# Optimization experiments

Measured on AMD Instinct MI355X. Metric: run time of the kernel, lower is better.

The kernel has to match this reference:

```python
import jax, jax.numpy as jnp
import numpy as np

D_MODEL = 1024
N_HEADS = 16
D_HEAD = D_MODEL // N_HEADS

def setup_inputs() -> dict:
    key = jax.random.key(0)
    ks = jax.random.split(key, 5)
    B, T = 4, 2048
    s = 1.0 / np.sqrt(D_MODEL)
    return {
        "x": jax.random.normal(ks[0], (B, T, D_MODEL), dtype=jnp.float32),
        "qkv_w": jax.random.normal(ks[1], (3 * D_MODEL, D_MODEL), dtype=jnp.float32) * s,
        "qkv_b": jnp.zeros((3 * D_MODEL,), dtype=jnp.float32),
        "out_w": jax.random.normal(ks[2], (D_MODEL, D_MODEL), dtype=jnp.float32) * s,
        "out_b": jnp.zeros((D_MODEL,), dtype=jnp.float32),
    }

def reference(x, qkv_w, qkv_b, out_w, out_b):
    B, T, D = x.shape
    # fused QKV projection: [B,T,3D] -> [3,B,H,T,dh]
    qkv = (x @ qkv_w.T + qkv_b).reshape(B, T, 3, N_HEADS, D_HEAD)
    qkv = jnp.transpose(qkv, (2, 0, 3, 1, 4))
    q, k, v = qkv[0], qkv[1], qkv[2]
    scale = 1.0 / np.sqrt(D_HEAD).astype(np.float32)
    scores = jnp.einsum("bhqd,bhkd->bhqk", q, k) * scale
    attn = jax.nn.softmax(scores, axis=-1)
    ctx = jnp.einsum("bhqk,bhkd->bhqd", attn, v)  # [B,H,T,dh]
    ctx = jnp.transpose(ctx, (0, 2, 1, 3)).reshape(B, T, D)
    return ctx @ out_w.T + out_b
```

## Files before the change

kernel.cpp:

```cpp
#include <hip/hip_runtime.h>
#include <hip/hip_bf16.h>
#include <cstdint>
#include <cstddef>


#define SEQ 2048
#define DM 1024

typedef __attribute__((ext_vector_type(8))) short bf16x8;
typedef __attribute__((ext_vector_type(4))) short bf16x4;
typedef __attribute__((ext_vector_type(4))) float f32x4;

static __device__ __forceinline__ short f2bf(float f) {
  union { float f; uint32_t u; } v; v.f = f;
  uint32_t r = v.u + 0x7fffu + ((v.u >> 16) & 1u);
  return (short)(r >> 16);
}

static __device__ __forceinline__ float exp2_native(float x) {
  return __builtin_amdgcn_exp2f(x);
}

typedef const __attribute__((address_space(1))) unsigned int* gas_ptr;
typedef __attribute__((address_space(3))) unsigned int* las_ptr;
static __device__ __forceinline__ void gl2lds16(const void* g, void* l) {
  __builtin_amdgcn_global_load_lds((gas_ptr)g, (las_ptr)l, 16, 0, 0);
}

static __device__ __forceinline__ unsigned permhi(float a_odd, float a_even) {
  union { float f; unsigned u; } x, y; x.f = a_odd; y.f = a_even;
  return __builtin_amdgcn_perm(x.u, y.u, 0x07060302u);
}
static __device__ __forceinline__ bf16x8 pack8t(const float* e) {
  union { bf16x8 v; unsigned u[4]; } r;
  r.u[0] = permhi(e[1], e[0]);
  r.u[1] = permhi(e[3], e[2]);
  r.u[2] = permhi(e[5], e[4]);
  r.u[3] = permhi(e[7], e[6]);
  return r.v;
}

static __device__ __forceinline__ int swz(int r) {
  return (r & 3) | (((r >> 3) & 1) << 2);
}

__global__ __launch_bounds__(256)
void cvt_bf16(const float* __restrict__ src, short* __restrict__ dst) {
  int i = blockIdx.x * 256 + threadIdx.x;
  float4 v = ((const float4*)src)[i];
  bf16x4 p = { f2bf(v.x), f2bf(v.y), f2bf(v.z), f2bf(v.w) };
  ((bf16x4*)dst)[i] = p;
}

__global__ __launch_bounds__(256)
void cvt_bf16_2(const float* __restrict__ src1, short* __restrict__ dst1, int n1,
                const float* __restrict__ src2, short* __restrict__ dst2) {
  int b = blockIdx.x;
  const float* s; short* d; int i;
  if (b < n1) { s = src1; d = dst1; i = b * 256 + threadIdx.x; }
  else        { s = src2; d = dst2; i = (b - n1) * 256 + threadIdx.x; }
  float4 v = ((const float4*)s)[i];
  bf16x4 p = { f2bf(v.x), f2bf(v.y), f2bf(v.z), f2bf(v.w) };
  ((bf16x4*)d)[i] = p;
}

__global__ __launch_bounds__(256)
void cvt_bf16_3(const float* __restrict__ src1, short* __restrict__ dst1, int n1,
                const float* __restrict__ src2, short* __restrict__ dst2, int n2,
                const float* __restrict__ src3, short* __restrict__ dst3) {
  int b = blockIdx.x;
  const float* s; short* d; int i;
  if (b < n1)           { s = src1; d = dst1; i = b * 256 + threadIdx.x; }
  else if (b < n1 + n2) { s = src2; d = dst2; i = (b - n1) * 256 + threadIdx.x; }
  else                  { s = src3; d = dst3; i = (b - n1 - n2) * 256 + threadIdx.x; }
  float4 v = ((const float4*)s)[i];
  bf16x4 p = { f2bf(v.x), f2bf(v.y), f2bf(v.z), f2bf(v.w) };
  ((bf16x4*)d)[i] = p;
}

__global__ __launch_bounds__(256, 2)
void qkv_gemm(const short* __restrict__ Xb, const short* __restrict__ Wb,
              const float* __restrict__ bias,
              short* __restrict__ Q, short* __restrict__ K,
              short* __restrict__ Vt) {
  __shared__ short As[2][128 * 64];
  __shared__ short Bs[2][128 * 64];
  const int tid  = threadIdx.x;
  const int m0   = blockIdx.x * 128;
  const int n0   = blockIdx.y * 128;
  const int lane = tid & 63;
  const int w    = tid >> 6;
  const int wm   = (w >> 1) * 64, wn = (w & 1) * 64;
  const int l15  = lane & 15, quad = lane >> 4;

  int g_row[4], g_col[4];
#pragma unroll
  for (int p = 0; p < 4; p++) {
    int r = p * 32 + w * 8 + (lane >> 3);
    g_row[p] = r;
    g_col[p] = ((lane & 7) ^ swz(r)) << 3;
  }
  int aoff[4][2], boff[4][2];
#pragma unroll
  for (int i = 0; i < 4; i++)
#pragma unroll
    for (int ks = 0; ks < 2; ks++) {
      int Ra = wm + i * 16 + l15;
      aoff[i][ks] = Ra * 128 + (((ks * 4 + quad) ^ swz(Ra)) << 4);
      int Rb = wn + i * 16 + l15;
      boff[i][ks] = Rb * 128 + (((ks * 4 + quad) ^ swz(Rb)) << 4);
    }

  f32x4 acc[4][4];
  for (int i = 0; i < 4; i++)
    for (int j = 0; j < 4; j++) acc[i][j] = (f32x4)0.0f;

#pragma unroll
  for (int p = 0; p < 4; p++) {
    gl2lds16(&Xb[(size_t)(m0 + g_row[p]) * DM + g_col[p]], &As[0][(p * 32 + w * 8) * 64]);
    gl2lds16(&Wb[(size_t)(n0 + g_row[p]) * DM + g_col[p]], &Bs[0][(p * 32 + w * 8) * 64]);
  }

  for (int t = 0; t < 16; t++) {
    const int cur = t & 1;
    if (t + 1 < 16) {
      const int kk = (t + 1) * 64;
#pragma unroll
      for (int p = 0; p < 4; p++) {
        gl2lds16(&Xb[(size_t)(m0 + g_row[p]) * DM + kk + g_col[p]], &As[cur ^ 1][(p * 32 + w * 8) * 64]);
        gl2lds16(&Wb[(size_t)(n0 + g_row[p]) * DM + kk + g_col[p]], &Bs[cur ^ 1][(p * 32 + w * 8) * 64]);
      }
      asm volatile("s_waitcnt vmcnt(8)" ::: "memory");
    } else {
      asm volatile("s_waitcnt vmcnt(0)" ::: "memory");
    }
    __builtin_amdgcn_s_barrier();
    __builtin_amdgcn_sched_barrier(0);

    const char* Ab = (const char*)&As[cur][0];
    const char* Bb = (const char*)&Bs[cur][0];
#pragma unroll
    for (int ks = 0; ks < 2; ks++) {
      bf16x8 af[4], bfr[4];
      for (int i = 0; i < 4; i++) af[i]  = *(const bf16x8*)(Ab + aoff[i][ks]);
      for (int j = 0; j < 4; j++) bfr[j] = *(const bf16x8*)(Bb + boff[j][ks]);
      for (int i = 0; i < 4; i++)
        for (int j = 0; j < 4; j++)
          acc[i][j] = __builtin_amdgcn_mfma_f32_16x16x32_bf16(af[i], bfr[j], acc[i][j], 0, 0, 0);
    }
    __builtin_amdgcn_sched_barrier(0);
    __builtin_amdgcn_s_barrier();
    __builtin_amdgcn_sched_barrier(0);
  }

  const float C1 = 0.18033688011112042f;
  const int qkv = n0 >> 10;
  for (int i = 0; i < 4; i++) {
    const int m = m0 + wm + i * 16 + quad * 4;
    const int bb = m >> 11, t = m & 2047;
    for (int j = 0; j < 4; j++) {
      const int f  = n0 + wn + j * 16 + l15;
      const int fi = f & 1023;
      const int h  = fi >> 6, d = fi & 63;
      const float bv = bias[f];
      if (qkv == 2) {
        bf16x4 pk = { f2bf(acc[i][j][0] + bv), f2bf(acc[i][j][1] + bv),
                      f2bf(acc[i][j][2] + bv), f2bf(acc[i][j][3] + bv) };
        *(bf16x4*)&Vt[((size_t)(bb * 16 + h) * 64 + d) * SEQ + t] = pk;
      } else {
        short* dst = (qkv == 0) ? Q : K;
        const float sc = (qkv == 0) ? C1 : 1.0f;
        size_t base = ((size_t)(bb * 16 + h) * SEQ + t) * 64 + d;
        for (int r = 0; r < 4; r++)
          dst[base + (size_t)r * 64] = f2bf((acc[i][j][r] + bv) * sc);
      }
    }
  }
}

__global__ __launch_bounds__(256, 4)
void attn(const short* __restrict__ Q, const short* __restrict__ K,
          const short* __restrict__ Vt, short* __restrict__ ctx) {
  __shared__ short Ks[2][64 * 64];
  __shared__ short Vs[2][64 * 64];
  const int tid  = threadIdx.x;
  const int w    = tid >> 6, lane = tid & 63;
  const int l15  = lane & 15, quad = lane >> 4;

  const int L    = blockIdx.y * 16 + blockIdx.x;
  const int m_   = L >> 3;
  const int bh   = ((m_ >> 4) << 3) | (L & 7);
  const int qr   = (m_ & 15) * 128 + w * 32;

  const short* Kb = &K[(size_t)bh * SEQ * 64];
  const short* Vb = &Vt[(size_t)bh * 64 * SEQ];

  const int kperm = (l15 >> 2) * 8 + (l15 & 3);

  int dr[2], dc[2];
#pragma unroll
  for (int p = 0; p < 2; p++) {
    int ci = p * 256 + w * 64 + lane;
    dr[p] = ci >> 3;
    dc[p] = (ci & 7) ^ swz(ci >> 3);
  }
  const short* kp[2];
  const short* vp[2];
#pragma unroll
  for (int p = 0; p < 2; p++) {
    kp[p] = &Kb[(size_t)(64 + dr[p]) * 64 + dc[p] * 8];
    vp[p] = &Vb[(size_t)dr[p] * SEQ + 64 + dc[p] * 8];
  }

  int koff[2][2][2][2];
  int voff[2][4][2];
#pragma unroll
  for (int blk = 0; blk < 2; blk++)
#pragma unroll
    for (int tau = 0; tau < 2; tau++)
#pragma unroll
      for (int ks = 0; ks < 2; ks++) {
        int R = blk * 32 + kperm + tau * 4;
        int c = (ks * 4 + quad) ^ swz(R);
        int off = (R * 8 + c) * 16;
        koff[0][blk][tau][ks] = off;
        koff[1][blk][tau][ks] = off + 8192;
      }
#pragma unroll
  for (int dt = 0; dt < 4; dt++)
#pragma unroll
    for (int blk = 0; blk < 2; blk++) {
      int R = dt * 16 + l15;
      int c = (blk * 4 + quad) ^ swz(R);
      int off = (R * 8 + c) * 16;
      voff[0][dt][blk] = off;
      voff[1][dt][blk] = off + 8192;
    }
  const char* KsB = (const char*)&Ks[0][0];
  const char* VsB = (const char*)&Vs[0][0];

  bf16x8 qf[2][2];
#pragma unroll
  for (int mt = 0; mt < 2; mt++)
#pragma unroll
    for (int ks = 0; ks < 2; ks++)
      qf[mt][ks] = *(const bf16x8*)&Q[(size_t)bh * SEQ * 64 + (size_t)(qr + mt * 16 + l15) * 64 + ks * 32 + quad * 8];

  f32x4 O[2][4];
#pragma unroll
  for (int mt = 0; mt < 2; mt++)
    for (int dt = 0; dt < 4; dt++) O[mt][dt] = (f32x4)0.0f;
  f32x4 psA[2];
  psA[0] = (f32x4)0.0f; psA[1] = (f32x4)0.0f;
  const short one_bf = (short)0x3F80;
  const bf16x8 ones = { one_bf, one_bf, one_bf, one_bf, one_bf, one_bf, one_bf, one_bf };

#pragma unroll
  for (int p = 0; p < 2; p++) {
    gl2lds16(&Kb[(size_t)dr[p] * 64 + dc[p] * 8],  &Ks[0][(p * 256 + w * 64) * 8]);
    gl2lds16(&Vb[(size_t)dr[p] * SEQ + dc[p] * 8], &Vs[0][(p * 256 + w * 64) * 8]);
  }
  __syncthreads();

  for (int k0 = 0; k0 < SEQ; k0 += 128) {
#pragma unroll
    for (int half = 0; half < 2; half++) {
      const bool doPf = (half == 0) || (k0 + 128 < SEQ);
      if (doPf) {
#pragma unroll
        for (int p = 0; p < 2; p++) {
          gl2lds16(kp[p], &Ks[half ^ 1][(p * 256 + w * 64) * 8]);
          gl2lds16(vp[p], &Vs[half ^ 1][(p * 256 + w * 64) * 8]);
        }
      }
#pragma unroll
      for (int p = 0; p < 2; p++) { kp[p] += 64 * 64; vp[p] += 64; }

      bf16x8 kf[2][2][2];
#pragma unroll
      for (int blk = 0; blk < 2; blk++)
#pragma unroll
        for (int tau = 0; tau < 2; tau++)
#pragma unroll
          for (int ks = 0; ks < 2; ks++)
            kf[blk][tau][ks] = *(const bf16x8*)(KsB + koff[half][blk][tau][ks]);

      f32x4 S[2][2][2];
#pragma unroll
      for (int mt = 0; mt < 2; mt++)
#pragma unroll
        for (int blk = 0; blk < 2; blk++) {
          f32x4 S0 = (f32x4)0.0f, S1 = (f32x4)0.0f;
#pragma unroll
          for (int ks = 0; ks < 2; ks++) {
            S0 = __builtin_amdgcn_mfma_f32_16x16x32_bf16(kf[blk][0][ks], qf[mt][ks], S0, 0, 0, 0);
            S1 = __builtin_amdgcn_mfma_f32_16x16x32_bf16(kf[blk][1][ks], qf[mt][ks], S1, 0, 0, 0);
          }
          S[mt][blk][0] = S0; S[mt][blk][1] = S1;
        }

      bf16x8 vf[4][2];
#pragma unroll
      for (int dt = 0; dt < 4; dt++)
#pragma unroll
        for (int blk = 0; blk < 2; blk++)
          vf[dt][blk] = *(const bf16x8*)(VsB + voff[half][dt][blk]);

      bf16x8 pp[2][2];
#pragma unroll
      for (int mt = 0; mt < 2; mt++)
#pragma unroll
        for (int blk = 0; blk < 2; blk++) {
          float e[8];
#pragma unroll
          for (int r = 0; r < 4; r++) {
            e[r]     = exp2_native(S[mt][blk][0][r]);
            e[4 + r] = exp2_native(S[mt][blk][1][r]);
          }
          pp[mt][blk] = pack8t(e);
        }

#pragma unroll
      for (int blk = 0; blk < 2; blk++) {
#pragma unroll
        for (int dt = 0; dt < 4; dt++) {
          O[0][dt] = __builtin_amdgcn_mfma_f32_16x16x32_bf16(vf[dt][blk], pp[0][blk], O[0][dt], 0, 0, 0);
          O[1][dt] = __builtin_amdgcn_mfma_f32_16x16x32_bf16(vf[dt][blk], pp[1][blk], O[1][dt], 0, 0, 0);
        }
        psA[0] = __builtin_amdgcn_mfma_f32_16x16x32_bf16(ones, pp[0][blk], psA[0], 0, 0, 0);
        psA[1] = __builtin_amdgcn_mfma_f32_16x16x32_bf16(ones, pp[1][blk], psA[1], 0, 0, 0);
      }

      __syncthreads();
    }
  }

  const int bb = bh >> 4, h = bh & 15;
#pragma unroll
  for (int mt = 0; mt < 2; mt++) {
    float rinv = 1.0f / psA[mt][0];
    const int t = qr + mt * 16 + l15;
#pragma unroll
    for (int dt = 0; dt < 4; dt++) {
      bf16x4 ov = { f2bf(O[mt][dt][0] * rinv), f2bf(O[mt][dt][1] * rinv),
                    f2bf(O[mt][dt][2] * rinv), f2bf(O[mt][dt][3] * rinv) };
      *(bf16x4*)&ctx[(size_t)(bb * SEQ + t) * DM + h * 64 + dt * 16 + quad * 4] = ov;
    }
  }
}

__global__ __launch_bounds__(256, 2)
void out_gemm(const short* __restrict__ Cx, const short* __restrict__ Ob,
              const float* __restrict__ bias, float* __restrict__ Y) {
  __shared__ short As[2][128 * 64];
  __shared__ short Bs[2][128 * 64];
  const int tid  = threadIdx.x;
  const int m0   = blockIdx.x * 128;
  const int n0   = blockIdx.y * 128;
  const int lane = tid & 63;
  const int w    = tid >> 6;
  const int wm   = (w >> 1) * 64, wn = (w & 1) * 64;
  const int l15  = lane & 15, quad = lane >> 4;

  int g_row[4], g_col[4];
#pragma unroll
  for (int p = 0; p < 4; p++) {
    int r = p * 32 + w * 8 + (lane >> 3);
    g_row[p] = r;
    g_col[p] = ((lane & 7) ^ swz(r)) << 3;
  }
  int aoff[4][2], boff[4][2];
#pragma unroll
  for (int i = 0; i < 4; i++)
#pragma unroll
    for (int ks = 0; ks < 2; ks++) {
      int Ra = wm + i * 16 + l15;
      aoff[i][ks] = Ra * 128 + (((ks * 4 + quad) ^ swz(Ra)) << 4);
      int Rb = wn + i * 16 + l15;
      boff[i][ks] = Rb * 128 + (((ks * 4 + quad) ^ swz(Rb)) << 4);
    }

  f32x4 acc[4][4];
  for (int i = 0; i < 4; i++)
    for (int j = 0; j < 4; j++) acc[i][j] = (f32x4)0.0f;

#pragma unroll
  for (int p = 0; p < 4; p++) {
    gl2lds16(&Cx[(size_t)(m0 + g_row[p]) * DM + g_col[p]], &As[0][(p * 32 + w * 8) * 64]);
    gl2lds16(&Ob[(size_t)(n0 + g_row[p]) * DM + g_col[p]], &Bs[0][(p * 32 + w * 8) * 64]);
  }

  for (int t = 0; t < 16; t++) {
    const int cur = t & 1;
    if (t + 1 < 16) {
      const int kk = (t + 1) * 64;
#pragma unroll
      for (int p = 0; p < 4; p++) {
        gl2lds16(&Cx[(size_t)(m0 + g_row[p]) * DM + kk + g_col[p]], &As[cur ^ 1][(p * 32 + w * 8) * 64]);
        gl2lds16(&Ob[(size_t)(n0 + g_row[p]) * DM + kk + g_col[p]], &Bs[cur ^ 1][(p * 32 + w * 8) * 64]);
      }
      asm volatile("s_waitcnt vmcnt(8)" ::: "memory");
    } else {
      asm volatile("s_waitcnt vmcnt(0)" ::: "memory");
    }
    __builtin_amdgcn_s_barrier();
    __builtin_amdgcn_sched_barrier(0);

    const char* Ab = (const char*)&As[cur][0];
    const char* Bb = (const char*)&Bs[cur][0];
#pragma unroll
    for (int ks = 0; ks < 2; ks++) {
      bf16x8 af[4], bfr[4];
      for (int i = 0; i < 4; i++) af[i]  = *(const bf16x8*)(Ab + aoff[i][ks]);
      for (int j = 0; j < 4; j++) bfr[j] = *(const bf16x8*)(Bb + boff[j][ks]);
      for (int i = 0; i < 4; i++)
        for (int j = 0; j < 4; j++)
          acc[i][j] = __builtin_amdgcn_mfma_f32_16x16x32_bf16(af[i], bfr[j], acc[i][j], 0, 0, 0);
    }
    __builtin_amdgcn_sched_barrier(0);
    __builtin_amdgcn_s_barrier();
    __builtin_amdgcn_sched_barrier(0);
  }

  for (int i = 0; i < 4; i++) {
    const int m = m0 + wm + i * 16 + quad * 4;
    for (int j = 0; j < 4; j++) {
      const int n = n0 + wn + j * 16 + l15;
      const float bv = bias[n];
      for (int r = 0; r < 4; r++)
        Y[(size_t)(m + r) * DM + n] = acc[i][j][r] + bv;
    }
  }
}

extern "C" void kernel_launch(void* const* d_in, const int* in_sizes, int n_in,
                              void* d_out, int out_size, void* d_ws, size_t ws_size,
                              hipStream_t stream) {
  const float* x     = (const float*)d_in[0];
  const float* qkv_w = (const float*)d_in[1];
  const float* qkv_b = (const float*)d_in[2];
  const float* out_w = (const float*)d_in[3];
  const float* out_b = (const float*)d_in[4];
  float* out = (float*)d_out;

  const size_t NBH = (size_t)4 * 16 * SEQ * 64;
  short* Q   = (short*)d_ws;
  short* K   = Q + NBH;
  short* Vt  = K + NBH;
  short* ctx = Vt + NBH;
  short* Xb  = ctx;
  short* Wb  = (short*)d_out;

  const size_t used  = 4 * NBH * sizeof(short);
  const size_t obsz  = (size_t)DM * DM * sizeof(short);
  const bool   bigws = ws_size >= used + obsz;

  if (bigws) {
    short* Ob = (short*)((char*)d_ws + used);
    cvt_bf16_3<<<dim3(8192 + 3072 + 1024), 256, 0, stream>>>(
        x, Xb, 8192, qkv_w, Wb, 3072, out_w, Ob);
    qkv_gemm<<<dim3(64, 24), 256, 0, stream>>>(Xb, Wb, qkv_b, Q, K, Vt);
    attn<<<dim3(SEQ / 128, 64), 256, 0, stream>>>(Q, K, Vt, ctx);
    out_gemm<<<dim3(64, 8), 256, 0, stream>>>(ctx, Ob, out_b, out);
  } else {
    short* Ob = Vt;
    cvt_bf16_2<<<dim3(8192 + 3072), 256, 0, stream>>>(x, Xb, 8192, qkv_w, Wb);
    qkv_gemm<<<dim3(64, 24), 256, 0, stream>>>(Xb, Wb, qkv_b, Q, K, Vt);
    attn<<<dim3(SEQ / 128, 64), 256, 0, stream>>>(Q, K, Vt, ctx);
    cvt_bf16<<<dim3(1024), 256, 0, stream>>>(out_w, Ob);
    out_gemm<<<dim3(64, 8), 256, 0, stream>>>(ctx, Ob, out_b, out);
  }
}
```

Before: 251.4 us.

## Deepen GEMM pipeline to four K=32 LDS stages with prefetch distance two

Both projection GEMMs switch from a double-buffered K=64 tile to a 4-buffer ring of K=32 tiles, prefetching two stages ahead with adjusted vmcnt waits and a new 4-chunk XOR swizzle. The aim is to hide global-to-LDS load latency better while keeping LDS usage the same. The cost is twice as many barriers per K and half the MFMA work between them, which can add synchronisation overhead.

```diff
diff --git a/kernel.cpp b/kernel.cpp
--- a/kernel.cpp
+++ b/kernel.cpp
@@ -83,8 +83,8 @@
               const float* __restrict__ bias,
               short* __restrict__ Q, short* __restrict__ K,
               short* __restrict__ Vt) {
-  __shared__ short As[2][128 * 64];
-  __shared__ short Bs[2][128 * 64];
+  __shared__ short As[4][128 * 32];
+  __shared__ short Bs[4][128 * 32];
   const int tid  = threadIdx.x;
   const int m0   = blockIdx.x * 128;
   const int n0   = blockIdx.y * 128;
@@ -93,61 +93,62 @@
   const int wm   = (w >> 1) * 64, wn = (w & 1) * 64;
   const int l15  = lane & 15, quad = lane >> 4;
 
-  int g_row[4], g_col[4];
-#pragma unroll
-  for (int p = 0; p < 4; p++) {
-    int r = p * 32 + w * 8 + (lane >> 3);
-    g_row[p] = r;
-    g_col[p] = ((lane & 7) ^ swz(r)) << 3;
-  }
-  int aoff[4][2], boff[4][2];
-#pragma unroll
-  for (int i = 0; i < 4; i++)
-#pragma unroll
-    for (int ks = 0; ks < 2; ks++) {
-      int Ra = wm + i * 16 + l15;
-      aoff[i][ks] = Ra * 128 + (((ks * 4 + quad) ^ swz(Ra)) << 4);
-      int Rb = wn + i * 16 + l15;
-      boff[i][ks] = Rb * 128 + (((ks * 4 + quad) ^ swz(Rb)) << 4);
-    }
+  int s_row[2], s_col[2];
+#pragma unroll
+  for (int p = 0; p < 2; p++) {
+    int ci = p * 256 + tid;
+    int r  = ci >> 2, cc = ci & 3;
+    s_row[p] = r;
+    s_col[p] = ((cc ^ (r & 3)) << 3);
+  }
+  int aoff[4], boff[4];
+#pragma unroll
+  for (int i = 0; i < 4; i++) {
+    int Ra = wm + i * 16 + l15;
+    aoff[i] = (Ra * 4 + (quad ^ (l15 & 3))) * 16;
+    int Rb = wn + i * 16 + l15;
+    boff[i] = (Rb * 4 + (quad ^ (l15 & 3))) * 16;
+  }
 
   f32x4 acc[4][4];
   for (int i = 0; i < 4; i++)
     for (int j = 0; j < 4; j++) acc[i][j] = (f32x4)0.0f;
 
 #pragma unroll
-  for (int p = 0; p < 4; p++) {
-    gl2lds16(&Xb[(size_t)(m0 + g_row[p]) * DM + g_col[p]], &As[0][(p * 32 + w * 8) * 64]);
-    gl2lds16(&Wb[(size_t)(n0 + g_row[p]) * DM + g_col[p]], &Bs[0][(p * 32 + w * 8) * 64]);
-  }
-
-  for (int t = 0; t < 16; t++) {
-    const int cur = t & 1;
-    if (t + 1 < 16) {
-      const int kk = (t + 1) * 64;
-#pragma unroll
-      for (int p = 0; p < 4; p++) {
-        gl2lds16(&Xb[(size_t)(m0 + g_row[p]) * DM + kk + g_col[p]], &As[cur ^ 1][(p * 32 + w * 8) * 64]);
-        gl2lds16(&Wb[(size_t)(n0 + g_row[p]) * DM + kk + g_col[p]], &Bs[cur ^ 1][(p * 32 + w * 8) * 64]);
+  for (int t = 0; t < 2; t++)
+#pragma unroll
+    for (int p = 0; p < 2; p++) {
+      gl2lds16(&Xb[(size_t)(m0 + s_row[p]) * DM + t * 32 + s_col[p]], &As[t][(p * 256 + w * 64) * 8]);
+      gl2lds16(&Wb[(size_t)(n0 + s_row[p]) * DM + t * 32 + s_col[p]], &Bs[t][(p * 256 + w * 64) * 8]);
+    }
+
+  for (int t = 0; t < 32; t++) {
+    const int b = t & 3;
+    if (t + 2 < 32) {
+      const int kk = (t + 2) * 32;
+      const int pb = (t + 2) & 3;
+#pragma unroll
+      for (int p = 0; p < 2; p++) {
+        gl2lds16(&Xb[(size_t)(m0 + s_row[p]) * DM + kk + s_col[p]], &As[pb][(p * 256 + w * 64) * 8]);
+        gl2lds16(&Wb[(size_t)(n0 + s_row[p]) * DM + kk + s_col[p]], &Bs[pb][(p * 256 + w * 64) * 8]);
       }
       asm volatile("s_waitcnt vmcnt(8)" ::: "memory");
+    } else if (t + 1 < 32) {
+      asm volatile("s_waitcnt vmcnt(4)" ::: "memory");
     } else {
       asm volatile("s_waitcnt vmcnt(0)" ::: "memory");
     }
     __builtin_amdgcn_s_barrier();
     __builtin_amdgcn_sched_barrier(0);
 
-    const char* Ab = (const char*)&As[cur][0];
-    const char* Bb = (const char*)&Bs[cur][0];
-#pragma unroll
-    for (int ks = 0; ks < 2; ks++) {
-      bf16x8 af[4], bfr[4];
-      for (int i = 0; i < 4; i++) af[i]  = *(const bf16x8*)(Ab + aoff[i][ks]);
-      for (int j = 0; j < 4; j++) bfr[j] = *(const bf16x8*)(Bb + boff[j][ks]);
-      for (int i = 0; i < 4; i++)
-        for (int j = 0; j < 4; j++)
-          acc[i][j] = __builtin_amdgcn_mfma_f32_16x16x32_bf16(af[i], bfr[j], acc[i][j], 0, 0, 0);
-    }
+    const char* Ab = (const char*)&As[b][0];
+    const char* Bb = (const char*)&Bs[b][0];
+    bf16x8 af[4], bfr[4];
+    for (int i = 0; i < 4; i++) af[i]  = *(const bf16x8*)(Ab + aoff[i]);
+    for (int j = 0; j < 4; j++) bfr[j] = *(const bf16x8*)(Bb + boff[j]);
+    for (int i = 0; i < 4; i++)
+      for (int j = 0; j < 4; j++)
+        acc[i][j] = __builtin_amdgcn_mfma_f32_16x16x32_bf16(af[i], bfr[j], acc[i][j], 0, 0, 0);
     __builtin_amdgcn_sched_barrier(0);
     __builtin_amdgcn_s_barrier();
     __builtin_amdgcn_sched_barrier(0);
@@ -352,8 +353,8 @@
 __global__ __launch_bounds__(256, 2)
 void out_gemm(const short* __restrict__ Cx, const short* __restrict__ Ob,
               const float* __restrict__ bias, float* __restrict__ Y) {
-  __shared__ short As[2][128 * 64];
-  __shared__ short Bs[2][128 * 64];
+  __shared__ short As[4][128 * 32];
+  __shared__ short Bs[4][128 * 32];
   const int tid  = threadIdx.x;
   const int m0   = blockIdx.x * 128;
   const int n0   = blockIdx.y * 128;
@@ -362,61 +363,62 @@
   const int wm   = (w >> 1) * 64, wn = (w & 1) * 64;
   const int l15  = lane & 15, quad = lane >> 4;
 
-  int g_row[4], g_col[4];
-#pragma unroll
-  for (int p = 0; p < 4; p++) {
-    int r = p * 32 + w * 8 + (lane >> 3);
-    g_row[p] = r;
-    g_col[p] = ((lane & 7) ^ swz(r)) << 3;
-  }
-  int aoff[4][2], boff[4][2];
-#pragma unroll
-  for (int i = 0; i < 4; i++)
-#pragma unroll
-    for (int ks = 0; ks < 2; ks++) {
-      int Ra = wm + i * 16 + l15;
-      aoff[i][ks] = Ra * 128 + (((ks * 4 + quad) ^ swz(Ra)) << 4);
-      int Rb = wn + i * 16 + l15;
-      boff[i][ks] = Rb * 128 + (((ks * 4 + quad) ^ swz(Rb)) << 4);
-    }
+  int s_row[2], s_col[2];
+#pragma unroll
+  for (int p = 0; p < 2; p++) {
+    int ci = p * 256 + tid;
+    int r  = ci >> 2, cc = ci & 3;
+    s_row[p] = r;
+    s_col[p] = ((cc ^ (r & 3)) << 3);
+  }
+  int aoff[4], boff[4];
+#pragma unroll
+  for (int i = 0; i < 4; i++) {
+    int Ra = wm + i * 16 + l15;
+    aoff[i] = (Ra * 4 + (quad ^ (l15 & 3))) * 16;
+    int Rb = wn + i * 16 + l15;
+    boff[i] = (Rb * 4 + (quad ^ (l15 & 3))) * 16;
+  }
 
   f32x4 acc[4][4];
   for (int i = 0; i < 4; i++)
     for (int j = 0; j < 4; j++) acc[i][j] = (f32x4)0.0f;
 
 #pragma unroll
-  for (int p = 0; p < 4; p++) {
-    gl2lds16(&Cx[(size_t)(m0 + g_row[p]) * DM + g_col[p]], &As[0][(p * 32 + w * 8) * 64]);
-    gl2lds16(&Ob[(size_t)(n0 + g_row[p]) * DM + g_col[p]], &Bs[0][(p * 32 + w * 8) * 64]);
-  }
-
-  for (int t = 0; t < 16; t++) {
-    const int cur = t & 1;
-    if (t + 1 < 16) {
-      const int kk = (t + 1) * 64;
-#pragma unroll
-      for (int p = 0; p < 4; p++) {
-        gl2lds16(&Cx[(size_t)(m0 + g_row[p]) * DM + kk + g_col[p]], &As[cur ^ 1][(p * 32 + w * 8) * 64]);
-        gl2lds16(&Ob[(size_t)(n0 + g_row[p]) * DM + kk + g_col[p]], &Bs[cur ^ 1][(p * 32 + w * 8) * 64]);
+  for (int t = 0; t < 2; t++)
+#pragma unroll
+    for (int p = 0; p < 2; p++) {
+      gl2lds16(&Cx[(size_t)(m0 + s_row[p]) * DM + t * 32 + s_col[p]], &As[t][(p * 256 + w * 64) * 8]);
+      gl2lds16(&Ob[(size_t)(n0 + s_row[p]) * DM + t * 32 + s_col[p]], &Bs[t][(p * 256 + w * 64) * 8]);
+    }
+
+  for (int t = 0; t < 32; t++) {
+    const int b = t & 3;
+    if (t + 2 < 32) {
+      const int kk = (t + 2) * 32;
+      const int pb = (t + 2) & 3;
+#pragma unroll
+      for (int p = 0; p < 2; p++) {
+        gl2lds16(&Cx[(size_t)(m0 + s_row[p]) * DM + kk + s_col[p]], &As[pb][(p * 256 + w * 64) * 8]);
+        gl2lds16(&Ob[(size_t)(n0 + s_row[p]) * DM + kk + s_col[p]], &Bs[pb][(p * 256 + w * 64) * 8]);
       }
       asm volatile("s_waitcnt vmcnt(8)" ::: "memory");
+    } else if (t + 1 < 32) {
+      asm volatile("s_waitcnt vmcnt(4)" ::: "memory");
     } else {
       asm volatile("s_waitcnt vmcnt(0)" ::: "memory");
     }
     __builtin_amdgcn_s_barrier();
     __builtin_amdgcn_sched_barrier(0);
 
-    const char* Ab = (const char*)&As[cur][0];
-    const char* Bb = (const char*)&Bs[cur][0];
-#pragma unroll
-    for (int ks = 0; ks < 2; ks++) {
-      bf16x8 af[4], bfr[4];
-      for (int i = 0; i < 4; i++) af[i]  = *(const bf16x8*)(Ab + aoff[i][ks]);
-      for (int j = 0; j < 4; j++) bfr[j] = *(const bf16x8*)(Bb + boff[j][ks]);
-      for (int i = 0; i < 4; i++)
-        for (int j = 0; j < 4; j++)
-          acc[i][j] = __builtin_amdgcn_mfma_f32_16x16x32_bf16(af[i], bfr[j], acc[i][j], 0, 0, 0);
-    }
+    const char* Ab = (const char*)&As[b][0];
+    const char* Bb = (const char*)&Bs[b][0];
+    bf16x8 af[4], bfr[4];
+    for (int i = 0; i < 4; i++) af[i]  = *(const bf16x8*)(Ab + aoff[i]);
+    for (int j = 0; j < 4; j++) bfr[j] = *(const bf16x8*)(Bb + boff[j]);
+    for (int i = 0; i < 4; i++)
+      for (int j = 0; j < 4; j++)
+        acc[i][j] = __builtin_amdgcn_mfma_f32_16x16x32_bf16(af[i], bfr[j], acc[i][j], 0, 0, 0);
     __builtin_amdgcn_sched_barrier(0);
     __builtin_amdgcn_s_barrier();
     __builtin_amdgcn_sched_barrier(0);
```

Result: slower. 274.5 us (+9.2%).
